# Kernel optimization log

Measured on AMD Instinct MI355X. Metric: run time of the kernel, lower is better.

The kernel has to match this reference:

```python
import jax, jax.numpy as jnp
import numpy as np

N_EXPERTS = 8
N_SHARED = 1
N_ROUTED = N_EXPERTS - N_SHARED          # 7
TOP_K_ROUTED = 3 - N_SHARED              # 2 routed experts per token
C = 1024
H = 4 * C


def _mlp(x, w_fc, w_proj):
    # x: [n, C]; w_fc: [C, H]; w_proj: [H, C]; exact (erf) GELU like torch nn.GELU
    return jax.nn.gelu(x @ w_fc, approximate=False) @ w_proj


def setup_inputs() -> dict:
    key = jax.random.key(0)
    ks = jax.random.split(key, 6)
    s = 0.02
    return {
        "x": jax.random.normal(ks[0], (4, 2048, C), dtype=jnp.float32),
        "gate_w": jax.random.normal(ks[1], (N_ROUTED, C), dtype=jnp.float32) * s,
        "lb_bias": jnp.zeros((N_ROUTED,), dtype=jnp.float32),
        "shared_wfc": jax.random.normal(ks[2], (C, H), dtype=jnp.float32) * s,
        "shared_wproj": jax.random.normal(ks[3], (H, C), dtype=jnp.float32) * s,
        "routed_wfc": jax.random.normal(ks[4], (N_ROUTED, C, H), dtype=jnp.float32) * s,
        "routed_wproj": jax.random.normal(ks[5], (N_ROUTED, H, C), dtype=jnp.float32) * s,
    }


def reference(x, gate_w, lb_bias, shared_wfc, shared_wproj, routed_wfc, routed_wproj):
    B, T, Cc = x.shape
    xt = x.reshape(-1, Cc)                       # [n, C]
    n = xt.shape[0]

    # shared expert(s) applied to every token
    shared_out = _mlp(xt, shared_wfc, shared_wproj)

    # routing
    routed_logits = xt @ gate_w.T                # [n, E_r]
    sel_logits = routed_logits + lb_bias
    _, topk_idx = jax.lax.top_k(sel_logits, TOP_K_ROUTED)   # [n, k]
    routed_probs = jax.nn.softmax(routed_logits.astype(jnp.float32), axis=-1)
    topk_w = jnp.take_along_axis(routed_probs, topk_idx, axis=-1)  # [n, k]

    # per-token combine weights over routed experts: [n, E_r]
    cw = jnp.zeros((n, N_ROUTED), dtype=jnp.float32)
    cw = cw.at[jnp.arange(n)[:, None], topk_idx].add(topk_w)

    # dispatch-combine: small fixed loop over routed experts
    routed_out = jnp.zeros_like(xt)
    for e in range(N_ROUTED):
        y = _mlp(xt, routed_wfc[e], routed_wproj[e])
        routed_out = routed_out + cw[:, e:e + 1] * y

    return (shared_out + routed_out).reshape(B, T, Cc)
```

## Files before the change

kernel.cpp:

```cpp
#include <hip/hip_runtime.h>
#include <hip/hip_bf16.h>

#define AS1 __attribute__((address_space(1)))
#define AS3 __attribute__((address_space(3)))

typedef __bf16 bf16x8 __attribute__((ext_vector_type(8)));
typedef float f32x4 __attribute__((ext_vector_type(4)));

static constexpr int C_DIM = 1024;
static constexpr int H_DIM = 4096;
static constexpr int NTOK  = 8192;
static constexpr int NR    = 7;
static constexpr int NSLOT = 17408;
static constexpr int MAXT  = 136;
static constexpr size_t WSZ = (size_t)C_DIM * H_DIM;

static __device__ __forceinline__ unsigned short f2bf(float f) {
  __hip_bfloat16 h = __float2bfloat16(f);
  return *reinterpret_cast<unsigned short*>(&h);
}
static __device__ __forceinline__ float bf2f(unsigned short u) {
  unsigned int v = ((unsigned int)u) << 16;
  return *reinterpret_cast<float*>(&v);
}

static __device__ __forceinline__ float gelu_fast(float v) {
  const float u2 = -2.0f * v * (0.7978845608f + 0.0356774081f * v * v);
  return v * __builtin_amdgcn_rcpf(1.0f + __expf(u2));
}

static __device__ __forceinline__ void gload16(const void* g, void* lds) {
  __builtin_amdgcn_global_load_lds((const AS1 void*)g, (AS3 void*)lds, 16, 0, 0);
}

static __device__ __forceinline__ void tile_decode(int f, int gx, int gy,
                                                   int& ty, int& bx) {
  const int myc = gy >> 3;
  const int xcd = f & 7;
  const int r = f >> 3;
  const int GM = 8;
  const int nig = GM * gx;
  const int grp = r / nig;
  const int first = grp * GM;
  const int gsz = min(GM, myc - first);
  const int rin = r - grp * nig;
  ty = xcd * myc + first + rin % gsz;
  bx = rin / gsz;
}

__global__ __launch_bounds__(256) void cast_x_kernel(const float* __restrict__ x,
                                                     unsigned short* __restrict__ xb) {
  size_t i = ((size_t)blockIdx.x * blockDim.x + threadIdx.x) * 4;
  float4 v = *(const float4*)(x + i);
  ushort4 o;
  o.x = f2bf(v.x); o.y = f2bf(v.y); o.z = f2bf(v.z); o.w = f2bf(v.w);
  *(ushort4*)(xb + i) = o;
}

__global__ __launch_bounds__(256) void init_kernel(int* __restrict__ idx, int* __restrict__ cnt,
                                                   int* __restrict__ cursor) {
  int i = blockIdx.x * 256 + threadIdx.x;
  if (i < NSLOT) idx[i] = 0;
  if (blockIdx.x == 0 && threadIdx.x < 8) { cnt[threadIdx.x] = 0; cursor[threadIdx.x] = 0; }
}

__global__ __launch_bounds__(256) void routing_kernel(const float* __restrict__ x,
                                                      const float* __restrict__ gw,
                                                      const float* __restrict__ bias,
                                                      float* __restrict__ cw,
                                                      int* __restrict__ cnt) {
  int wid = (int)((blockIdx.x * (size_t)blockDim.x + threadIdx.x) >> 6);
  int lane = threadIdx.x & 63;
  if (wid >= NTOK) return;
  const float* xt = x + (size_t)wid * C_DIM;
  float p[NR] = {0.f, 0.f, 0.f, 0.f, 0.f, 0.f, 0.f};
  for (int i = lane; i < C_DIM; i += 64) {
    float xv = xt[i];
#pragma unroll
    for (int e = 0; e < NR; ++e) p[e] += xv * gw[e * C_DIM + i];
  }
#pragma unroll
  for (int e = 0; e < NR; ++e) {
#pragma unroll
    for (int off = 32; off; off >>= 1) p[e] += __shfl_down(p[e], off);
  }
  if (lane == 0) {
    float m = p[0];
#pragma unroll
    for (int e = 1; e < NR; ++e) m = fmaxf(m, p[e]);
    float pr[NR], s = 0.f;
#pragma unroll
    for (int e = 0; e < NR; ++e) { pr[e] = __expf(p[e] - m); s += pr[e]; }
    float inv = 1.0f / s;
#pragma unroll
    for (int e = 0; e < NR; ++e) pr[e] *= inv;
    float sel[NR];
#pragma unroll
    for (int e = 0; e < NR; ++e) sel[e] = p[e] + bias[e];
    int i1 = 0;
#pragma unroll
    for (int e = 1; e < NR; ++e) if (sel[e] > sel[i1]) i1 = e;
    int i2 = -1;
#pragma unroll
    for (int e = 0; e < NR; ++e) {
      if (e == i1) continue;
      if (i2 < 0 || sel[e] > sel[i2]) i2 = e;
    }
    float c[NR] = {0.f, 0.f, 0.f, 0.f, 0.f, 0.f, 0.f};
    c[i1] = pr[i1];
    c[i2] += pr[i2];
#pragma unroll
    for (int e = 0; e < NR; ++e) cw[(size_t)wid * NR + e] = c[e];
    atomicAdd(&cnt[i1], 1);
    atomicAdd(&cnt[i2], 1);
  }
}

__global__ void scan_kernel(const int* __restrict__ cnt, int* __restrict__ offs,
                            int* __restrict__ tmap, int* __restrict__ ntiles) {
  int o = 0, nt = 0;
  for (int e = 0; e < NR; ++e) {
    offs[e] = o;
    int n = (cnt[e] + 127) & ~127;
    o += n;
    for (int tm = 0; tm < n; tm += 128) tmap[nt++] = (e << 16) | tm;
  }
  *ntiles = nt;
}

__global__ __launch_bounds__(256) void place_kernel(const float* __restrict__ cw,
                                                    const int* __restrict__ offs,
                                                    int* __restrict__ cursor,
                                                    int* __restrict__ idx,
                                                    int* __restrict__ tok2slot,
                                                    float* __restrict__ tok2w) {
  int t = blockIdx.x * 256 + threadIdx.x;
  if (t >= NTOK) return;
  int k = 0;
#pragma unroll
  for (int e = 0; e < NR; ++e) {
    float w = cw[(size_t)t * NR + e];
    if (w > 0.f) {
      int p = atomicAdd(&cursor[e], 1);
      int slot = offs[e] + p;
      idx[slot] = t;
      tok2slot[t * 2 + k] = slot;
      tok2w[t * 2 + k] = w;
      ++k;
    }
  }
}

__global__ void transpose_cast_all(const float* __restrict__ shared_w,
                                   const float* __restrict__ routed_w,
                                   unsigned short* __restrict__ out, int R, int S) {
  int e = blockIdx.z;
  const float* in = (e == 0) ? shared_w : routed_w + (size_t)(e - 1) * R * S;
  unsigned short* o = out + (size_t)e * R * S;
  __shared__ float t[32][33];
  int bx = blockIdx.x * 32;
  int by = blockIdx.y * 32;
  int tx = threadIdx.x, ty = threadIdx.y;
#pragma unroll
  for (int i = 0; i < 32; i += 8)
    t[ty + i][tx] = in[(size_t)(by + ty + i) * S + bx + tx];
  __syncthreads();
#pragma unroll
  for (int i = 0; i < 32; i += 8)
    o[(size_t)(bx + ty + i) * R + by + tx] = f2bf(t[tx][ty + i]);
}


template <bool GATHER>
__global__ __launch_bounds__(256) void gemm_fc(const unsigned short* __restrict__ A,
                                               const unsigned short* __restrict__ BtAll,
                                               unsigned short* __restrict__ Y,
                                               const int* __restrict__ idx,
                                               const int* __restrict__ offs,
                                               const int* __restrict__ tmap,
                                               const int* __restrict__ ntiles) {
  __shared__ __align__(16) unsigned short As[3][4800];
  __shared__ __align__(16) unsigned short Bs[3][4800];
  const int tid = threadIdx.x;
  const int wave = tid >> 6, lane = tid & 63;
  constexpr int NT = C_DIM / 32;

  int bx, ty;
  {
    const int f = blockIdx.y * gridDim.x + blockIdx.x;
    tile_decode(f, gridDim.x, gridDim.y, ty, bx);
  }

  int m0, n0, base;
  const unsigned short* Bt;
  if (GATHER) {
    if (ty >= *ntiles) return;
    const int packed = tmap[ty];
    const int e = packed >> 16;
    m0 = packed & 0xffff;
    n0 = bx * 128;
    base = offs[e];
    Bt = BtAll + (size_t)(e + 1) * WSZ;
  } else {
    m0 = ty * 128;
    n0 = bx * 128;
    base = 0;
    Bt = BtAll;
  }

  const int q0 = wave * 128 + lane, q1 = q0 + 64;
  const int kg0 = q0 >> 7, r0 = q0 & 127;
  const int kg1 = q1 >> 7, r1 = q1 & 127;
  const size_t rowA0 = GATHER ? (size_t)idx[base + m0 + r0] : (size_t)(m0 + r0);
  const size_t rowA1 = GATHER ? (size_t)idx[base + m0 + r1] : (size_t)(m0 + r1);
  const unsigned short* gA0 = A + rowA0 * C_DIM + kg0 * 8;
  const unsigned short* gA1 = A + rowA1 * C_DIM + kg1 * 8;
  const unsigned short* gB0 = Bt + (size_t)(n0 + r0) * C_DIM + kg0 * 8;
  const unsigned short* gB1 = Bt + (size_t)(n0 + r1) * C_DIM + kg1 * 8;
  const int c0 = (wave * 2 + 0) * 512, c1 = (wave * 2 + 1) * 512;

  const int wr = wave >> 1, wc = wave & 1;
  const int fr = lane & 15, fq = lane >> 4;
  f32x4 acc[4][4] = {};

  asm volatile("s_waitcnt vmcnt(0)" ::: "memory");
  gload16(gA0, &As[0][c0]); gload16(gA1, &As[0][c1]);
  gload16(gB0, &Bs[0][c0]); gload16(gB1, &Bs[0][c1]);
  gload16(gA0 + 32, &As[1][c0]); gload16(gA1 + 32, &As[1][c1]);
  gload16(gB0 + 32, &Bs[1][c0]); gload16(gB1 + 32, &Bs[1][c1]);

  int rb = 0;
  for (int t = 0; t < NT; ++t) {
    if (t + 2 < NT) {
      const int wb = (rb >= 1) ? rb - 1 : 2;
      const int nk = (t + 2) * 32;
      gload16(gA0 + nk, &As[wb][c0]); gload16(gA1 + nk, &As[wb][c1]);
      gload16(gB0 + nk, &Bs[wb][c0]); gload16(gB1 + nk, &Bs[wb][c1]);
      asm volatile("s_waitcnt vmcnt(8)" ::: "memory");
    } else if (t + 1 < NT) {
      asm volatile("s_waitcnt vmcnt(4)" ::: "memory");
    } else {
      asm volatile("s_waitcnt vmcnt(0)" ::: "memory");
    }
    __builtin_amdgcn_s_barrier();
    bf16x8 af[4], bfr[4];
#pragma unroll
    for (int m = 0; m < 4; ++m)
      af[m] = *(const bf16x8*)&As[rb][fq * 1024 + (wr * 64 + m * 16 + fr) * 8];
#pragma unroll
    for (int n = 0; n < 4; ++n)
      bfr[n] = *(const bf16x8*)&Bs[rb][fq * 1024 + (wc * 64 + n * 16 + fr) * 8];
#pragma unroll
    for (int m = 0; m < 4; ++m)
#pragma unroll
      for (int n = 0; n < 4; ++n)
        acc[m][n] = __builtin_amdgcn_mfma_f32_16x16x32_bf16(af[m], bfr[n], acc[m][n], 0, 0, 0);
    __builtin_amdgcn_s_barrier();
    rb = (rb == 2) ? 0 : rb + 1;
  }

#pragma unroll
  for (int m = 0; m < 4; ++m)
#pragma unroll
    for (int n = 0; n < 4; ++n)
#pragma unroll
      for (int j = 0; j < 4; ++j) {
        const int row = m0 + wr * 64 + m * 16 + fq * 4 + j;
        const int col = n0 + wc * 64 + n * 16 + fr;
        const float g = gelu_fast(acc[m][n][j]);
        Y[(size_t)(base + row) * H_DIM + col] = f2bf(g);
      }
}

__global__ __launch_bounds__(256) void gemm_proj_shared(const unsigned short* __restrict__ Yg,
                                                        const unsigned short* __restrict__ Bt,
                                                        float* __restrict__ Out) {
  __shared__ __align__(16) unsigned short As[3][4096];
  __shared__ __align__(16) unsigned short Bs[3][4096];
  const int tid = threadIdx.x;
  const int wave = tid >> 6, lane = tid & 63;
  constexpr int NT = H_DIM / 32;

  int bx, ty;
  {
    const int f = blockIdx.y * gridDim.x + blockIdx.x;
    tile_decode(f, gridDim.x, gridDim.y, ty, bx);
  }
  const int m0 = ty * 128;
  const int n0 = bx * 128;

  const int q0 = wave * 128 + lane, q1 = q0 + 64;
  const int kg0 = q0 >> 7, r0 = q0 & 127;
  const int kg1 = q1 >> 7, r1 = q1 & 127;
  const unsigned short* gA0 = Yg + (size_t)(m0 + r0) * H_DIM + kg0 * 8;
  const unsigned short* gA1 = Yg + (size_t)(m0 + r1) * H_DIM + kg1 * 8;
  const unsigned short* gB0 = Bt + (size_t)(n0 + r0) * H_DIM + kg0 * 8;
  const unsigned short* gB1 = Bt + (size_t)(n0 + r1) * H_DIM + kg1 * 8;
  const int c0 = (wave * 2 + 0) * 512, c1 = (wave * 2 + 1) * 512;

  const int wr = wave >> 1, wc = wave & 1;
  const int fr = lane & 15, fq = lane >> 4;
  f32x4 acc[4][4] = {};

  gload16(gA0, &As[0][c0]); gload16(gA1, &As[0][c1]);
  gload16(gB0, &Bs[0][c0]); gload16(gB1, &Bs[0][c1]);
  gload16(gA0 + 32, &As[1][c0]); gload16(gA1 + 32, &As[1][c1]);
  gload16(gB0 + 32, &Bs[1][c0]); gload16(gB1 + 32, &Bs[1][c1]);

  int rb = 0;
  for (int t = 0; t < NT; ++t) {
    if (t + 2 < NT) {
      const int wb = (rb >= 1) ? rb - 1 : 2;
      const int nk = (t + 2) * 32;
      gload16(gA0 + nk, &As[wb][c0]); gload16(gA1 + nk, &As[wb][c1]);
      gload16(gB0 + nk, &Bs[wb][c0]); gload16(gB1 + nk, &Bs[wb][c1]);
      asm volatile("s_waitcnt vmcnt(8)" ::: "memory");
    } else if (t + 1 < NT) {
      asm volatile("s_waitcnt vmcnt(4)" ::: "memory");
    } else {
      asm volatile("s_waitcnt vmcnt(0)" ::: "memory");
    }
    __builtin_amdgcn_s_barrier();
    bf16x8 af[4], bfr[4];
#pragma unroll
    for (int m = 0; m < 4; ++m)
      af[m] = *(const bf16x8*)&As[rb][fq * 1024 + (wr * 64 + m * 16 + fr) * 8];
#pragma unroll
    for (int n = 0; n < 4; ++n)
      bfr[n] = *(const bf16x8*)&Bs[rb][fq * 1024 + (wc * 64 + n * 16 + fr) * 8];
#pragma unroll
    for (int m = 0; m < 4; ++m)
#pragma unroll
      for (int n = 0; n < 4; ++n)
        acc[m][n] = __builtin_amdgcn_mfma_f32_16x16x32_bf16(af[m], bfr[n], acc[m][n], 0, 0, 0);
    __builtin_amdgcn_s_barrier();
    rb = (rb == 2) ? 0 : rb + 1;
  }

#pragma unroll
  for (int m = 0; m < 4; ++m)
#pragma unroll
    for (int n = 0; n < 4; ++n)
#pragma unroll
      for (int j = 0; j < 4; ++j) {
        const int p = wr * 64 + m * 16 + fq * 4 + j;
        const int col = n0 + wc * 64 + n * 16 + fr;
        Out[(size_t)(m0 + p) * C_DIM + col] = acc[m][n][j];
      }
}

__global__ __launch_bounds__(256) void gemm_proj_routed(const unsigned short* __restrict__ Yg,
                                                        const unsigned short* __restrict__ BtAll,
                                                        unsigned short* __restrict__ Pb,
                                                        const int* __restrict__ offs,
                                                        const int* __restrict__ tmap,
                                                        const int* __restrict__ ntiles) {
  __shared__ __align__(16) unsigned short As[3][4096];
  __shared__ __align__(16) unsigned short Bs[3][4096];
  const int tid = threadIdx.x;
  const int wave = tid >> 6, lane = tid & 63;
  constexpr int KSEG = H_DIM / 2;
  constexpr int NT = KSEG / 32;
  const int kbase = blockIdx.z * KSEG;

  int bx, ty;
  {
    const int f = blockIdx.y * gridDim.x + blockIdx.x;
    tile_decode(f, gridDim.x, gridDim.y, ty, bx);
  }

  if (ty >= *ntiles) return;
  const int packed = tmap[ty];
  const int e = packed >> 16;
  const int m0 = packed & 0xffff;
  const int n0 = bx * 128;
  const int base = offs[e];
  const unsigned short* Bt = BtAll + (size_t)(e + 1) * WSZ;

  const int q0 = wave * 128 + lane, q1 = q0 + 64;
  const int kg0 = q0 >> 7, r0 = q0 & 127;
  const int kg1 = q1 >> 7, r1 = q1 & 127;
  const unsigned short* gA0 = Yg + (size_t)(base + m0 + r0) * H_DIM + kbase + kg0 * 8;
  const unsigned short* gA1 = Yg + (size_t)(base + m0 + r1) * H_DIM + kbase + kg1 * 8;
  const unsigned short* gB0 = Bt + (size_t)(n0 + r0) * H_DIM + kbase + kg0 * 8;
  const unsigned short* gB1 = Bt + (size_t)(n0 + r1) * H_DIM + kbase + kg1 * 8;
  const int c0 = (wave * 2 + 0) * 512, c1 = (wave * 2 + 1) * 512;

  const int wr = wave >> 1, wc = wave & 1;
  const int fr = lane & 15, fq = lane >> 4;
  f32x4 acc[4][4] = {};

  gload16(gA0, &As[0][c0]); gload16(gA1, &As[0][c1]);
  gload16(gB0, &Bs[0][c0]); gload16(gB1, &Bs[0][c1]);
  gload16(gA0 + 32, &As[1][c0]); gload16(gA1 + 32, &As[1][c1]);
  gload16(gB0 + 32, &Bs[1][c0]); gload16(gB1 + 32, &Bs[1][c1]);

  int rb = 0;
  for (int t = 0; t < NT; ++t) {
    if (t + 2 < NT) {
      const int wb = (rb >= 1) ? rb - 1 : 2;
      const int nk = (t + 2) * 32;
      gload16(gA0 + nk, &As[wb][c0]); gload16(gA1 + nk, &As[wb][c1]);
      gload16(gB0 + nk, &Bs[wb][c0]); gload16(gB1 + nk, &Bs[wb][c1]);
      asm volatile("s_waitcnt vmcnt(8)" ::: "memory");
    } else if (t + 1 < NT) {
      asm volatile("s_waitcnt vmcnt(4)" ::: "memory");
    } else {
      asm volatile("s_waitcnt vmcnt(0)" ::: "memory");
    }
    __builtin_amdgcn_s_barrier();
    bf16x8 af[4], bfr[4];
#pragma unroll
    for (int m = 0; m < 4; ++m)
      af[m] = *(const bf16x8*)&As[rb][fq * 1024 + (wr * 64 + m * 16 + fr) * 8];
#pragma unroll
    for (int n = 0; n < 4; ++n)
      bfr[n] = *(const bf16x8*)&Bs[rb][fq * 1024 + (wc * 64 + n * 16 + fr) * 8];
#pragma unroll
    for (int m = 0; m < 4; ++m)
#pragma unroll
      for (int n = 0; n < 4; ++n)
        acc[m][n] = __builtin_amdgcn_mfma_f32_16x16x32_bf16(af[m], bfr[n], acc[m][n], 0, 0, 0);
    __builtin_amdgcn_s_barrier();
    rb = (rb == 2) ? 0 : rb + 1;
  }

#pragma unroll
  for (int m = 0; m < 4; ++m)
#pragma unroll
    for (int n = 0; n < 4; ++n)
#pragma unroll
      for (int j = 0; j < 4; ++j) {
        const int p = wr * 64 + m * 16 + fq * 4 + j;
        const int col = n0 + wc * 64 + n * 16 + fr;
        __builtin_nontemporal_store(
            f2bf(acc[m][n][j]),
            &Pb[((size_t)blockIdx.z * NSLOT + base + m0 + p) * C_DIM + col]);
      }
}

__global__ __launch_bounds__(256) void combine_kernel(const unsigned short* __restrict__ P,
                                                      const int* __restrict__ tok2slot,
                                                      const float* __restrict__ tok2w,
                                                      float* __restrict__ out) {
  const int t = blockIdx.x;
  const int c = threadIdx.x * 4;
  const int s0 = tok2slot[t * 2], s1 = tok2slot[t * 2 + 1];
  const float w0 = tok2w[t * 2], w1 = tok2w[t * 2 + 1];
  const ushort4 a0 = *(const ushort4*)&P[((size_t)0 * NSLOT + s0) * C_DIM + c];
  const ushort4 a1 = *(const ushort4*)&P[((size_t)1 * NSLOT + s0) * C_DIM + c];
  const ushort4 b0 = *(const ushort4*)&P[((size_t)0 * NSLOT + s1) * C_DIM + c];
  const ushort4 b1 = *(const ushort4*)&P[((size_t)1 * NSLOT + s1) * C_DIM + c];
  float4 o = *(float4*)&out[(size_t)t * C_DIM + c];
  o.x += w0 * (bf2f(a0.x) + bf2f(a1.x)) + w1 * (bf2f(b0.x) + bf2f(b1.x));
  o.y += w0 * (bf2f(a0.y) + bf2f(a1.y)) + w1 * (bf2f(b0.y) + bf2f(b1.y));
  o.z += w0 * (bf2f(a0.z) + bf2f(a1.z)) + w1 * (bf2f(b0.z) + bf2f(b1.z));
  o.w += w0 * (bf2f(a0.w) + bf2f(a1.w)) + w1 * (bf2f(b0.w) + bf2f(b1.w));
  *(float4*)&out[(size_t)t * C_DIM + c] = o;
}

extern "C" void kernel_launch(void* const* d_in, const int* in_sizes, int n_in,
                              void* d_out, int out_size, void* d_ws, size_t ws_size,
                              hipStream_t stream) {
  const float* x            = (const float*)d_in[0];
  const float* gate_w       = (const float*)d_in[1];
  const float* lb_bias      = (const float*)d_in[2];
  const float* shared_wfc   = (const float*)d_in[3];
  const float* shared_wproj = (const float*)d_in[4];
  const float* routed_wfc   = (const float*)d_in[5];
  const float* routed_wproj = (const float*)d_in[6];
  float* out = (float*)d_out;

  char* ws = (char*)d_ws;
  unsigned short* xb     = (unsigned short*)(ws);
  unsigned short* wfcT   = (unsigned short*)(ws + 16777216);
  unsigned short* Pb     = (unsigned short*)(ws);
  unsigned short* wprojT = (unsigned short*)(ws + 83886080);
  unsigned short* Yg     = (unsigned short*)(ws + 150994944);
  float*          cw     = (float*)(ws + 293601280);
  int*            idx    = (int*)(ws + 293830656);
  int*            cnt    = (int*)(ws + 293901312);
  int*            offs   = (int*)(ws + 293901376);
  int*            cursor = (int*)(ws + 293901440);
  int*            tok2slot = (int*)(ws + 293901504);
  float*          tok2w    = (float*)(ws + 293967040);
  int*            tmap     = (int*)(ws + 294032576);
  int*            ntiles   = (int*)(ws + 294033152);

  cast_x_kernel<<<NTOK * C_DIM / (256 * 4), 256, 0, stream>>>(x, xb);
  init_kernel<<<(NSLOT + 255) / 256, 256, 0, stream>>>(idx, cnt, cursor);
  routing_kernel<<<NTOK / 4, 256, 0, stream>>>(x, gate_w, lb_bias, cw, cnt);
  scan_kernel<<<1, 1, 0, stream>>>(cnt, offs, tmap, ntiles);
  place_kernel<<<NTOK / 256, 256, 0, stream>>>(cw, offs, cursor, idx, tok2slot, tok2w);

  transpose_cast_all<<<dim3(H_DIM / 32, C_DIM / 32, 8), dim3(32, 8), 0, stream>>>(
      shared_wfc, routed_wfc, wfcT, C_DIM, H_DIM);
  transpose_cast_all<<<dim3(C_DIM / 32, H_DIM / 32, 8), dim3(32, 8), 0, stream>>>(
      shared_wproj, routed_wproj, wprojT, H_DIM, C_DIM);

  gemm_fc<false><<<dim3(H_DIM / 128, NTOK / 128), 256, 0, stream>>>(
      xb, wfcT, Yg, idx, offs, tmap, ntiles);
  gemm_proj_shared<<<dim3(C_DIM / 128, NTOK / 128), 256, 0, stream>>>(Yg, wprojT, out);

  gemm_fc<true><<<dim3(H_DIM / 128, MAXT), 256, 0, stream>>>(
      xb, wfcT, Yg, idx, offs, tmap, ntiles);
  gemm_proj_routed<<<dim3(C_DIM / 128, MAXT, 2), 256, 0, stream>>>(
      Yg, wprojT, Pb, offs, tmap, ntiles);

  combine_kernel<<<NTOK, 256, 0, stream>>>(Pb, tok2slot, tok2w, out);
}
```

Measured before the change: 1.285 ms.

## Double-buffer fc GEMM with BK=64 instead of triple-buffered BK=32

Changes the fc GEMM's shared-memory pipeline from three stages of K=32 to two stages of K=64. Each iteration now issues 8 async global-to-LDS loads and runs 32 MFMAs per barrier pair. The aim is to halve the barrier and loop overhead per unit of work and improve the ratio of MFMA to synchronisation. In exchange the prefetch depth drops to a single stage ahead, LDS use rises, and the original padded layout (4800 entries per buffer) becomes unpadded (8192), which may add bank conflicts.

After: 1.312 ms. +2.2%, slower.

```diff
diff --git a/kernel.cpp b/kernel.cpp
--- a/kernel.cpp
+++ b/kernel.cpp
@@ -170,7 +170,6 @@
     o[(size_t)(bx + ty + i) * R + by + tx] = f2bf(t[tx][ty + i]);
 }
 
-
 template <bool GATHER>
 __global__ __launch_bounds__(256) void gemm_fc(const unsigned short* __restrict__ A,
                                                const unsigned short* __restrict__ BtAll,
@@ -179,11 +178,11 @@
                                                const int* __restrict__ offs,
                                                const int* __restrict__ tmap,
                                                const int* __restrict__ ntiles) {
-  __shared__ __align__(16) unsigned short As[3][4800];
-  __shared__ __align__(16) unsigned short Bs[3][4800];
+  __shared__ __align__(16) unsigned short As[2][8192];
+  __shared__ __align__(16) unsigned short Bs[2][8192];
   const int tid = threadIdx.x;
   const int wave = tid >> 6, lane = tid & 63;
-  constexpr int NT = C_DIM / 32;
+  constexpr int NT = C_DIM / 64;
 
   int bx, ty;
   {
@@ -208,55 +207,59 @@
     Bt = BtAll;
   }
 
-  const int q0 = wave * 128 + lane, q1 = q0 + 64;
-  const int kg0 = q0 >> 7, r0 = q0 & 127;
-  const int kg1 = q1 >> 7, r1 = q1 & 127;
-  const size_t rowA0 = GATHER ? (size_t)idx[base + m0 + r0] : (size_t)(m0 + r0);
-  const size_t rowA1 = GATHER ? (size_t)idx[base + m0 + r1] : (size_t)(m0 + r1);
-  const unsigned short* gA0 = A + rowA0 * C_DIM + kg0 * 8;
-  const unsigned short* gA1 = A + rowA1 * C_DIM + kg1 * 8;
-  const unsigned short* gB0 = Bt + (size_t)(n0 + r0) * C_DIM + kg0 * 8;
-  const unsigned short* gB1 = Bt + (size_t)(n0 + r1) * C_DIM + kg1 * 8;
-  const int c0 = (wave * 2 + 0) * 512, c1 = (wave * 2 + 1) * 512;
+  const int srow = (wave & 1) * 64 + lane;
+  const int kgb = wave >> 1;
+  const size_t rowA = GATHER ? (size_t)idx[base + m0 + srow] : (size_t)(m0 + srow);
+  const unsigned short* gA = A + rowA * C_DIM + kgb * 8;
+  const unsigned short* gB = Bt + (size_t)(n0 + srow) * C_DIM + kgb * 8;
+  const int dbase = kgb * 1024 + (wave & 1) * 512;
 
   const int wr = wave >> 1, wc = wave & 1;
   const int fr = lane & 15, fq = lane >> 4;
   f32x4 acc[4][4] = {};
 
   asm volatile("s_waitcnt vmcnt(0)" ::: "memory");
-  gload16(gA0, &As[0][c0]); gload16(gA1, &As[0][c1]);
-  gload16(gB0, &Bs[0][c0]); gload16(gB1, &Bs[0][c1]);
-  gload16(gA0 + 32, &As[1][c0]); gload16(gA1 + 32, &As[1][c1]);
-  gload16(gB0 + 32, &Bs[1][c0]); gload16(gB1 + 32, &Bs[1][c1]);
+#pragma unroll
+  for (int i = 0; i < 4; ++i) {
+    gload16(gA + i * 16, &As[0][dbase + i * 2048]);
+    gload16(gB + i * 16, &Bs[0][dbase + i * 2048]);
+  }
 
   int rb = 0;
   for (int t = 0; t < NT; ++t) {
-    if (t + 2 < NT) {
-      const int wb = (rb >= 1) ? rb - 1 : 2;
-      const int nk = (t + 2) * 32;
-      gload16(gA0 + nk, &As[wb][c0]); gload16(gA1 + nk, &As[wb][c1]);
-      gload16(gB0 + nk, &Bs[wb][c0]); gload16(gB1 + nk, &Bs[wb][c1]);
+    if (t + 1 < NT) {
+      const int wb = rb ^ 1;
+      const int nk = (t + 1) * 64;
+#pragma unroll
+      for (int i = 0; i < 4; ++i) {
+        gload16(gA + nk + i * 16, &As[wb][dbase + i * 2048]);
+        gload16(gB + nk + i * 16, &Bs[wb][dbase + i * 2048]);
+      }
       asm volatile("s_waitcnt vmcnt(8)" ::: "memory");
-    } else if (t + 1 < NT) {
-      asm volatile("s_waitcnt vmcnt(4)" ::: "memory");
     } else {
       asm volatile("s_waitcnt vmcnt(0)" ::: "memory");
     }
     __builtin_amdgcn_s_barrier();
-    bf16x8 af[4], bfr[4];
+    bf16x8 af[4][2], bfr[4][2];
 #pragma unroll
     for (int m = 0; m < 4; ++m)
-      af[m] = *(const bf16x8*)&As[rb][fq * 1024 + (wr * 64 + m * 16 + fr) * 8];
+#pragma unroll
+      for (int ks = 0; ks < 2; ++ks)
+        af[m][ks] = *(const bf16x8*)&As[rb][(ks * 4 + fq) * 1024 + (wr * 64 + m * 16 + fr) * 8];
 #pragma unroll
     for (int n = 0; n < 4; ++n)
-      bfr[n] = *(const bf16x8*)&Bs[rb][fq * 1024 + (wc * 64 + n * 16 + fr) * 8];
+#pragma unroll
+      for (int ks = 0; ks < 2; ++ks)
+        bfr[n][ks] = *(const bf16x8*)&Bs[rb][(ks * 4 + fq) * 1024 + (wc * 64 + n * 16 + fr) * 8];
 #pragma unroll
     for (int m = 0; m < 4; ++m)
 #pragma unroll
       for (int n = 0; n < 4; ++n)
-        acc[m][n] = __builtin_amdgcn_mfma_f32_16x16x32_bf16(af[m], bfr[n], acc[m][n], 0, 0, 0);
+#pragma unroll
+        for (int ks = 0; ks < 2; ++ks)
+          acc[m][n] = __builtin_amdgcn_mfma_f32_16x16x32_bf16(af[m][ks], bfr[n][ks], acc[m][n], 0, 0, 0);
     __builtin_amdgcn_s_barrier();
-    rb = (rb == 2) ? 0 : rb + 1;
+    rb ^= 1;
   }
 
 #pragma unroll
```
